# Optimization experiments

Hardware: AMD Instinct MI355X
Metric: run time of the kernel (lower is better)

Reference implementation:

```python
import jax, jax.numpy as jnp
import numpy as np

# ---- Cl(4,1) geometric-product Cayley table: gp(a,b)[k] = a[i] b[j] C[i,j,k] ----
def _build_cayley():
    metric = np.array([1.0, 1.0, 1.0, 1.0, -1.0], dtype=np.float32)  # signature (4,1)
    C = np.zeros((32, 32, 32), dtype=np.float32)
    for a in range(32):
        for b in range(32):
            # canonical reordering sign (count of swaps to merge blades)
            cnt = 0
            ash = a >> 1
            while ash:
                cnt += bin(ash & b).count('1')
                ash >>= 1
            s = -1.0 if (cnt & 1) else 1.0
            common = a & b
            for i in range(5):
                if (common >> i) & 1:
                    s *= metric[i]
            C[a, b, a ^ b] = s
    return C

CAYLEY = _build_cayley()
N_HEADS = 8

def gp_cl41(a, b, C):
    # a, b: (..., 32) multivectors
    return jnp.einsum('...i,...j,ijk->...k', a, b, C)

def normalize_cl41(x, eps=1e-6):
    n = jnp.sqrt(jnp.sum(x * x, axis=-1, keepdims=True) + eps)
    return x / n

def vlinear(x, w, b):
    # x: (..., Din, 32), w: (Dout, Din), b: (Dout, 32) -- blade-wise channel mixing
    return jnp.einsum('...ik,oi->...ok', x, w) + b

def layernorm2d(x, w, b, eps=1e-5):
    # normalized_shape = [D, 32]
    m = jnp.mean(x, axis=(-2, -1), keepdims=True)
    v = jnp.var(x, axis=(-2, -1), keepdims=True)
    return (x - m) / jnp.sqrt(v + eps) * w + b

def attention(x, wq, bq, wk, bk, wv, bv, wo, bo):
    B, S, D, K = x.shape
    hd = D // N_HEADS
    q = vlinear(x, wq, bq).reshape(B, S, N_HEADS, hd, K)
    k = vlinear(x, wk, bk).reshape(B, S, N_HEADS, hd, K)
    v = vlinear(x, wv, bv).reshape(B, S, N_HEADS, hd, K)
    scores = jnp.einsum('bqhdk,bshdk->bhqs', q, k) / jnp.sqrt(jnp.float32(hd * K))
    p = jax.nn.softmax(scores, axis=-1)
    o = jnp.einsum('bhqs,bshdk->bqhdk', p, v).reshape(B, S, D, K)
    return vlinear(o, wo, bo)


def setup_inputs() -> dict:
    key = jax.random.key(0)
    B, S, D, K = 4, 512, 256, 32
    L, E, NC = 2, 4, 1000
    ks = jax.random.split(key, 24)
    s = 1.0 / np.sqrt(D)
    inp = {
        'x': jax.random.normal(ks[0], (B, S, D, K), jnp.float32),
        'ln1_w': jnp.ones((L, D, K), jnp.float32),
        'ln1_b': jnp.zeros((L, D, K), jnp.float32),
        'wq': jax.random.normal(ks[1], (L, D, D), jnp.float32) * s,
        'bq': jnp.zeros((L, D, K), jnp.float32),
        'wk': jax.random.normal(ks[2], (L, D, D), jnp.float32) * s,
        'bk': jnp.zeros((L, D, K), jnp.float32),
        'wv': jax.random.normal(ks[3], (L, D, D), jnp.float32) * s,
        'bv': jnp.zeros((L, D, K), jnp.float32),
        'wo': jax.random.normal(ks[4], (L, D, D), jnp.float32) * s,
        'bo': jnp.zeros((L, D, K), jnp.float32),
        'ln2_w': jnp.ones((L, D, K), jnp.float32),
        'ln2_b': jnp.zeros((L, D, K), jnp.float32),
        'w1': jax.random.normal(ks[5], (L, E * D, D), jnp.float32) * s,
        'b1': jnp.zeros((L, E * D, K), jnp.float32),
        'w2': jax.random.normal(ks[6], (L, D, E * D), jnp.float32) * (1.0 / np.sqrt(E * D)),
        'b2': jnp.zeros((L, D, K), jnp.float32),
        'wr': jax.random.normal(ks[7], (D, D), jnp.float32) * s,
        'br': jnp.zeros((D, K), jnp.float32),
        'wc': jax.random.normal(ks[8], (NC, D * K), jnp.float32) * 0.02,
        'bc': jnp.zeros((NC,), jnp.float32),
    }
    return inp


def reference(x, ln1_w, ln1_b, wq, bq, wk, bk, wv, bv, wo, bo,
              ln2_w, ln2_b, w1, b1, w2, b2, wr, br, wc, bc):
    C = jnp.asarray(CAYLEY)
    L = ln1_w.shape[0]
    for l in range(L):
        h = layernorm2d(x, ln1_w[l], ln1_b[l])
        x = x + attention(h, wq[l], bq[l], wk[l], bk[l], wv[l], bv[l], wo[l], bo[l])
        x = normalize_cl41(x)
        h = layernorm2d(x, ln2_w[l], ln2_b[l])
        h = jnp.tanh(vlinear(h, w1[l], b1[l]))
        x = x + vlinear(h, w2[l], b2[l])
        x = normalize_cl41(x)
    # Recursive Rotor Accumulator pooling: psi_{t+1} = normalize(gp(r_t, psi_t))
    delta = vlinear(x, wr, br)                    # (B, S, D, 32)
    B, S, D, K = delta.shape
    psi0 = jnp.zeros((B, D, K), x.dtype).at[..., 0].set(1.0)
    def step(psi, r_t):
        return normalize_cl41(gp_cl41(r_t, psi, C)), None
    psi, _ = jax.lax.scan(step, psi0, jnp.moveaxis(delta, 1, 0))
    logits = psi.reshape(B, D * K) @ wc.T + bc
    return logits
```

## Files before the change

### kernel.cpp

```cpp
#include <hip/hip_runtime.h>
#include <hip/hip_bf16.h>
#include <cstdint>
#include <cstddef>

typedef __bf16 bf16_t;
typedef __attribute__((ext_vector_type(8))) __bf16 bf16x8;
typedef __attribute__((ext_vector_type(4))) __bf16 bf16x4;
typedef __attribute__((ext_vector_type(4))) float f32x4;

#define DEV __device__ __forceinline__

DEV void async16(const bf16_t* g, bf16_t* l) {
  __builtin_amdgcn_global_load_lds((const __attribute__((address_space(1))) void*)g,
                                   (__attribute__((address_space(3))) void*)l, 16, 0, 0);
}

DEV float fast_tanh(float x) {
  const float ex = __expf(2.f * x);
  return 1.f - 2.f / (ex + 1.f);
}

enum { EPI_RESID = 0, EPI_FFN1 = 1, EPI_QKV = 2, EPI_SCORE = 3, EPI_PV = 4, EPI_DELTAT = 5 };

template<int EPI, bool TRANSB>
__global__ __launch_bounds__(256, 2)
void gemm_k(const bf16_t* __restrict__ A, const bf16_t* __restrict__ A2,
            const bf16_t* __restrict__ B, const bf16_t* __restrict__ B2,
            const float* __restrict__ bias, void* __restrict__ outp, void* __restrict__ outp2,
            int Kd, int lda, int ldb, long aStride, long bStride)
{
  __shared__ bf16_t sA [2][4096];
  __shared__ bf16_t sB [2][4096];
  __shared__ bf16_t sA2[2][4096];
  __shared__ bf16_t sB2[2][4096];

  const int tid  = threadIdx.x;
  const int lane = tid & 63;
  const int wv   = tid >> 6;
  const int wr   = wv >> 1, wc = wv & 1;

  unsigned gx = gridDim.x, gy = gridDim.y;
  unsigned nb = gx * gy * gridDim.z;
  unsigned fid = blockIdx.x + gx * (blockIdx.y + gy * blockIdx.z);
  if ((nb & 7u) == 0u) fid = (fid & 7u) * (nb >> 3) + (fid >> 3);
  const unsigned bxu = fid % gx;
  const unsigned rem = fid / gx;
  const unsigned byu = rem % gy;
  const unsigned bzu = rem / gy;
  const int m0 = byu * 128;
  const int n0 = bxu * 128;
  const int bz = bzu;

  const bf16_t *Ab, *Bb, *A2b, *B2b;
  if constexpr (EPI == EPI_SCORE) {
    const int h = bz & 7;
    const long ho = (long)(bz >> 3) * 512;
    Ab  = A  + (long)h * aStride + ho;
    Bb  = B  + (long)h * bStride + ho;
    A2b = A2 + (long)h * aStride + ho;
    B2b = B2 + (long)h * bStride + ho;
  } else {
    Ab  = A  + (long)bz * aStride;
    Bb  = B  + (long)bz * bStride;
    A2b = A2 + (long)bz * aStride;
    B2b = B2 + (long)bz * bStride;
  }

  const int sRow = tid >> 2;
  const int sKo  = (tid & 3) * 8;
  const int tr = tid & 15;
  const int tc = tid >> 4;

  f32x4 acc[4][4];
#pragma unroll
  for (int i = 0; i < 4; i++)
#pragma unroll
    for (int j = 0; j < 4; j++) acc[i][j] = f32x4{0.f, 0.f, 0.f, 0.f};

  const int ns  = Kd >> 5;
  const int off = (int)(fid & (unsigned)(ns - 1));

  uint4 br0, br1, br2, br3;

  auto stageA = [&](int si, int b) {
    const int kt = ((si + off) & (ns - 1)) << 5;
    const bf16_t* ga  = Ab  + (long)(m0 + sRow) * lda + kt + sKo;
    const bf16_t* ga2 = A2b + (long)(m0 + sRow) * lda + kt + sKo;
    async16(ga,             &sA [b][tid * 8]);
    async16(ga + 64 * lda,  &sA [b][2048 + tid * 8]);
    async16(ga2,            &sA2[b][tid * 8]);
    async16(ga2 + 64 * lda, &sA2[b][2048 + tid * 8]);
  };
  auto stageB = [&](int si, int b) {
    const int kt = ((si + off) & (ns - 1)) << 5;
    const bf16_t* gb  = Bb  + (long)(n0 + sRow) * ldb + kt + sKo;
    const bf16_t* gb2 = B2b + (long)(n0 + sRow) * ldb + kt + sKo;
    async16(gb,             &sB [b][tid * 8]);
    async16(gb + 64 * ldb,  &sB [b][2048 + tid * 8]);
    async16(gb2,            &sB2[b][tid * 8]);
    async16(gb2 + 64 * ldb, &sB2[b][2048 + tid * 8]);
  };
  auto loadBR = [&](int si) {
    const int kt = ((si + off) & (ns - 1)) << 5;
    const bf16_t* gb  = Bb  + (long)(kt + tr) * ldb + n0 + tc * 8;
    const bf16_t* gb2 = B2b + (long)(kt + tr) * ldb + n0 + tc * 8;
    br0 = *(const uint4*)gb;
    br1 = *(const uint4*)(gb + 16 * ldb);
    br2 = *(const uint4*)gb2;
    br3 = *(const uint4*)(gb2 + 16 * ldb);
  };

  stageA(0, 0);
  if constexpr (!TRANSB) stageB(0, 0); else loadBR(0);

  for (int si = 0; si < ns; si++) {
    const int cb = si & 1;
    if (si + 1 < ns) stageA(si + 1, cb ^ 1);
    if constexpr (TRANSB) {
      const bf16_t* e0 = (const bf16_t*)&br0;
      const bf16_t* e1 = (const bf16_t*)&br1;
      const bf16_t* e2 = (const bf16_t*)&br2;
      const bf16_t* e3 = (const bf16_t*)&br3;
#pragma unroll
      for (int j = 0; j < 8; j++) {
        sB [cb][(tc * 8 + j) * 32 + tr]      = e0[j];
        sB [cb][(tc * 8 + j) * 32 + tr + 16] = e1[j];
        sB2[cb][(tc * 8 + j) * 32 + tr]      = e2[j];
        sB2[cb][(tc * 8 + j) * 32 + tr + 16] = e3[j];
      }
      if (si + 1 < ns) loadBR(si + 1);
      if (si + 1 >= ns) asm volatile("s_waitcnt vmcnt(0)" ::: "memory");
    } else {
      if (si + 1 < ns) {
        stageB(si + 1, cb ^ 1);
        asm volatile("s_waitcnt vmcnt(8)" ::: "memory");
      } else {
        asm volatile("s_waitcnt vmcnt(0)" ::: "memory");
      }
    }
    __syncthreads();

    bf16x8 af[4], bfr[4], af2[4], bf2[4];
#pragma unroll
    for (int i = 0; i < 4; i++) {
      const int ao = (wr * 64 + i * 16 + (lane & 15)) * 32 + (lane >> 4) * 8;
      const int bo = (wc * 64 + i * 16 + (lane & 15)) * 32 + (lane >> 4) * 8;
      af[i]  = *(const bf16x8*)&sA [cb][ao];
      af2[i] = *(const bf16x8*)&sA2[cb][ao];
      bfr[i] = *(const bf16x8*)&sB [cb][bo];
      bf2[i] = *(const bf16x8*)&sB2[cb][bo];
    }
#pragma unroll
    for (int i = 0; i < 4; i++)
#pragma unroll
      for (int j = 0; j < 4; j++) {
        acc[i][j] = __builtin_amdgcn_mfma_f32_16x16x32_bf16(af[i],  bfr[j], acc[i][j], 0, 0, 0);
        acc[i][j] = __builtin_amdgcn_mfma_f32_16x16x32_bf16(af[i],  bf2[j], acc[i][j], 0, 0, 0);
        acc[i][j] = __builtin_amdgcn_mfma_f32_16x16x32_bf16(af2[i], bfr[j], acc[i][j], 0, 0, 0);
      }
    __syncthreads();
  }

  const int cn = lane & 15;
  const int rg = (lane >> 4) * 4;
#pragma unroll
  for (int i = 0; i < 4; i++) {
    const int mb = m0 + wr * 64 + i * 16 + rg;
#pragma unroll
    for (int j = 0; j < 4; j++) {
      const int n = n0 + wc * 64 + j * 16 + cn;
#pragma unroll
      for (int r = 0; r < 4; r++) {
        const int m = mb + r;
        const float v = acc[i][j][r];
        if constexpr (EPI == EPI_RESID) {
          const float bb = bias ? bias[n * 32 + (m & 31)] : 0.f;
          ((float*)outp)[(long)m * 256 + n] += v + bb;
        } else if constexpr (EPI == EPI_QKV) {
          const int s = m >> 5, kb = m & 31;
          const int proj = n >> 8, col = n & 255;
          const int h = col >> 5, dd = col & 31;
          const long oidx = (long)proj * 4194304 + (long)(h * 512 + s) * 1024 + kb * 32 + dd;
          const float t = v + bias[n * 32 + kb];
          const bf16_t hh = (bf16_t)t;
          ((bf16_t*)outp)[oidx]  = hh;
          ((bf16_t*)outp2)[oidx] = (bf16_t)(t - (float)hh);
        } else if constexpr (EPI == EPI_SCORE) {
          const int h = bz & 7, half = bz >> 3;
          float* dst = half ? (float*)outp2 : (float*)outp;
          dst[(long)h * 262144 + (long)m * 512 + n] = v * (1.f / 32.f);
        } else if constexpr (EPI == EPI_PV) {
          const int kb = n >> 5, dd = n & 31;
          const long oidx = (long)(m * 32 + kb) * 256 + bz * 32 + dd;
          const bf16_t hh = (bf16_t)v;
          ((bf16_t*)outp)[oidx]  = hh;
          ((bf16_t*)outp2)[oidx] = (bf16_t)(v - (float)hh);
        } else {
          const int b = m >> 14, t = (m >> 5) & 511, kb = m & 31;
          ((float*)outp)[(((long)(b * 256 + n) * 512 + t) * 32) + kb] = v + bias[n * 32 + kb];
        }
      }
    }
  }
}

__global__ __launch_bounds__(256, 2)
void ffn_k(const bf16_t* __restrict__ Ah, const bf16_t* __restrict__ Al,
           const bf16_t* __restrict__ W1h_, const bf16_t* __restrict__ W1l_,
           const bf16_t* __restrict__ W2h_, const bf16_t* __restrict__ W2l_,
           const float* __restrict__ b1, const float* __restrict__ b2,
           float* __restrict__ XT)
{
  __shared__ bf16_t sAh[32 * 256], sAl[32 * 256];
  __shared__ bf16_t sHh[32 * 136], sHl[32 * 136];

  const int tid  = threadIdx.x;
  const int lane = tid & 63;
  const int wn   = tid >> 6;
  const int l15  = lane & 15;
  const int lg   = lane >> 4;
  const int m0   = blockIdx.x * 32;
  const int coff = blockIdx.x & 7;
  const int soff = (blockIdx.x >> 3) & 7;
  const int toff = (blockIdx.x >> 3) & 3;

#pragma unroll
  for (int r = 0; r < 4; r++) {
    const int idx = r * 256 + tid;
    const int row = idx >> 5, cp = idx & 31;
    const int c = cp ^ (row & 31);
    async16(Ah + (long)(m0 + row) * 256 + c * 8, sAh + idx * 8);
    async16(Al + (long)(m0 + row) * 256 + c * 8, sAl + idx * 8);
  }
  asm volatile("s_waitcnt vmcnt(0)" ::: "memory");
  __syncthreads();

  f32x4 acc2[2][4];
#pragma unroll
  for (int i = 0; i < 2; i++)
#pragma unroll
    for (int j = 0; j < 4; j++) acc2[i][j] = f32x4{0.f, 0.f, 0.f, 0.f};

#pragma unroll 1
  for (int cc = 0; cc < 8; cc++) {
    const int ch = (cc + coff) & 7;
    const bf16_t* W1h = W1h_ + (long)(ch * 128) * 256;
    const bf16_t* W1l = W1l_ + (long)(ch * 128) * 256;

    f32x4 acc1[2][2];
#pragma unroll
    for (int i = 0; i < 2; i++)
#pragma unroll
      for (int j = 0; j < 2; j++) acc1[i][j] = f32x4{0.f, 0.f, 0.f, 0.f};

#pragma unroll 2
    for (int s = 0; s < 8; s++) {
      const int sp = (s + soff) & 7;
      bf16x8 a_h[2], a_l[2], w_h[2], w_l[2];
#pragma unroll
      for (int i = 0; i < 2; i++) {
        const int arow = i * 16 + l15;
        const int ac = (sp * 4 + lg) ^ (arow & 31);
        a_h[i] = *(const bf16x8*)&sAh[arow * 256 + ac * 8];
        a_l[i] = *(const bf16x8*)&sAl[arow * 256 + ac * 8];
      }
#pragma unroll
      for (int j = 0; j < 2; j++) {
        const int nrow = wn * 32 + j * 16 + l15;
        w_h[j] = *(const bf16x8*)(W1h + (long)nrow * 256 + sp * 32 + lg * 8);
        w_l[j] = *(const bf16x8*)(W1l + (long)nrow * 256 + sp * 32 + lg * 8);
      }
#pragma unroll
      for (int i = 0; i < 2; i++)
#pragma unroll
        for (int j = 0; j < 2; j++) {
          acc1[i][j] = __builtin_amdgcn_mfma_f32_16x16x32_bf16(w_h[j], a_h[i], acc1[i][j], 0, 0, 0);
          acc1[i][j] = __builtin_amdgcn_mfma_f32_16x16x32_bf16(w_h[j], a_l[i], acc1[i][j], 0, 0, 0);
          acc1[i][j] = __builtin_amdgcn_mfma_f32_16x16x32_bf16(w_l[j], a_h[i], acc1[i][j], 0, 0, 0);
        }
    }

#pragma unroll
    for (int i = 0; i < 2; i++) {
      const int m = i * 16 + l15;
      const int kb = (m0 + m) & 31;
#pragma unroll
      for (int j = 0; j < 2; j++) {
        const int nb4 = wn * 32 + j * 16 + lg * 4;
        bf16x4 h4, l4;
#pragma unroll
        for (int rr = 0; rr < 4; rr++) {
          const int n = nb4 + rr;
          const float t = fast_tanh(acc1[i][j][rr] + b1[(ch * 128 + n) * 32 + kb]);
          const bf16_t hh = (bf16_t)t;
          h4[rr] = hh;
          l4[rr] = (bf16_t)(t - (float)hh);
        }
        *(bf16x4*)&sHh[m * 136 + nb4] = h4;
        *(bf16x4*)&sHl[m * 136 + nb4] = l4;
      }
    }
    __syncthreads();

#pragma unroll 2
    for (int t = 0; t < 4; t++) {
      const int tp = (t + toff) & 3;
      bf16x8 h_h[2], h_l[2], v_h[4], v_l[4];
#pragma unroll
      for (int i = 0; i < 2; i++) {
        const int hrow = i * 16 + l15;
        h_h[i] = *(const bf16x8*)&sHh[hrow * 136 + tp * 32 + lg * 8];
        h_l[i] = *(const bf16x8*)&sHl[hrow * 136 + tp * 32 + lg * 8];
      }
#pragma unroll
      for (int j = 0; j < 4; j++) {
        const int n2 = wn * 64 + j * 16 + l15;
        v_h[j] = *(const bf16x8*)(W2h_ + (long)n2 * 1024 + ch * 128 + tp * 32 + lg * 8);
        v_l[j] = *(const bf16x8*)(W2l_ + (long)n2 * 1024 + ch * 128 + tp * 32 + lg * 8);
      }
#pragma unroll
      for (int i = 0; i < 2; i++)
#pragma unroll
        for (int j = 0; j < 4; j++) {
          acc2[i][j] = __builtin_amdgcn_mfma_f32_16x16x32_bf16(h_h[i], v_h[j], acc2[i][j], 0, 0, 0);
          acc2[i][j] = __builtin_amdgcn_mfma_f32_16x16x32_bf16(h_h[i], v_l[j], acc2[i][j], 0, 0, 0);
          acc2[i][j] = __builtin_amdgcn_mfma_f32_16x16x32_bf16(h_l[i], v_h[j], acc2[i][j], 0, 0, 0);
        }
    }
    __syncthreads();
  }

#pragma unroll
  for (int i = 0; i < 2; i++)
#pragma unroll
    for (int j = 0; j < 4; j++) {
      const int n2 = wn * 64 + j * 16 + l15;
#pragma unroll
      for (int rr = 0; rr < 4; rr++) {
        const int m = m0 + i * 16 + lg * 4 + rr;
        XT[(long)m * 256 + n2] += acc2[i][j][rr] + b2[n2 * 32 + (m & 31)];
      }
    }
}

__global__ __launch_bounds__(256)
void transpose_k(const float* __restrict__ src, float* __restrict__ dst, int R, int C)
{
  __shared__ float t[32][33];
  const long boff = (long)blockIdx.z * R * C;
  const int r0 = blockIdx.y * 32, c0 = blockIdx.x * 32;
  const int tx = threadIdx.x & 31, ty = threadIdx.x >> 5;
#pragma unroll
  for (int i = 0; i < 32; i += 8)
    t[ty + i][tx] = src[boff + (long)(r0 + ty + i) * C + c0 + tx];
  __syncthreads();
#pragma unroll
  for (int i = 0; i < 32; i += 8)
    dst[boff + (long)(c0 + ty + i) * R + r0 + tx] = t[tx][ty + i];
}

DEV void hilo4(const f32x4 t, bf16x4& h, bf16x4& l) {
#pragma unroll
  for (int j = 0; j < 4; j++) {
    const bf16_t hh = (bf16_t)t[j];
    h[j] = hh;
    l[j] = (bf16_t)(t[j] - (float)hh);
  }
}

template<int MODE>
__global__ __launch_bounds__(256)
void nl_k(const float* __restrict__ X, float* __restrict__ Xo,
          const float* __restrict__ wT, const float* __restrict__ bT,
          bf16_t* __restrict__ oh, bf16_t* __restrict__ ol)
{
  const int row = blockIdx.x * 4 + (threadIdx.x >> 6);
  const int l   = threadIdx.x & 63;
  const float4* Xr = (const float4*)X + (long)row * 2048 + l;
  f32x4 v[32];
#pragma unroll
  for (int kb = 0; kb < 32; kb++) {
    const float4 t = Xr[kb * 64];
    v[kb] = f32x4{t.x, t.y, t.z, t.w};
  }
  if constexpr (MODE & 1) {
    f32x4 ss = f32x4{1e-6f, 1e-6f, 1e-6f, 1e-6f};
#pragma unroll
    for (int kb = 0; kb < 32; kb++) ss += v[kb] * v[kb];
    const f32x4 rs = f32x4{rsqrtf(ss[0]), rsqrtf(ss[1]), rsqrtf(ss[2]), rsqrtf(ss[3])};
#pragma unroll
    for (int kb = 0; kb < 32; kb++) v[kb] *= rs;
    if constexpr (MODE & 2) {
      float4* Xw = (float4*)Xo + (long)row * 2048 + l;
#pragma unroll
      for (int kb = 0; kb < 32; kb++)
        Xw[kb * 64] = float4{v[kb][0], v[kb][1], v[kb][2], v[kb][3]};
    }
  }
  if constexpr (MODE & 4) {
    float s = 0.f, s2 = 0.f;
#pragma unroll
    for (int kb = 0; kb < 32; kb++) {
      s  += (v[kb][0] + v[kb][1]) + (v[kb][2] + v[kb][3]);
      s2 += (v[kb][0] * v[kb][0] + v[kb][1] * v[kb][1]) +
            (v[kb][2] * v[kb][2] + v[kb][3] * v[kb][3]);
    }
#pragma unroll
    for (int o = 32; o > 0; o >>= 1) { s += __shfl_xor(s, o); s2 += __shfl_xor(s2, o); }
    const float mean = s * (1.f / 8192.f);
    const float var  = s2 * (1.f / 8192.f) - mean * mean;
    const float rstd = rsqrtf(var + 1e-5f);
    const float4* w4 = (const float4*)wT + l;
    const float4* b4 = (const float4*)bT + l;
#pragma unroll
    for (int kb = 0; kb < 32; kb++) {
      const float4 ww = w4[kb * 64];
      const float4 bb = b4[kb * 64];
      f32x4 t;
      t[0] = (v[kb][0] - mean) * rstd * ww.x + bb.x;
      t[1] = (v[kb][1] - mean) * rstd * ww.y + bb.y;
      t[2] = (v[kb][2] - mean) * rstd * ww.z + bb.z;
      t[3] = (v[kb][3] - mean) * rstd * ww.w + bb.w;
      bf16x4 h4, l4;
      hilo4(t, h4, l4);
      const long oi = (long)row * 8192 + kb * 256 + l * 4;
      *(bf16x4*)&oh[oi] = h4;
      *(bf16x4*)&ol[oi] = l4;
    }
  }
  if constexpr (MODE & 8) {
#pragma unroll
    for (int kb = 0; kb < 32; kb++) {
      bf16x4 h4, l4;
      hilo4(v[kb], h4, l4);
      const long oi = (long)row * 8192 + kb * 256 + l * 4;
      *(bf16x4*)&oh[oi] = h4;
      *(bf16x4*)&ol[oi] = l4;
    }
  }
}

__global__ __launch_bounds__(256)
void softmax_k(const float* __restrict__ SC, const float* __restrict__ SC2,
               bf16_t* __restrict__ Ph, bf16_t* __restrict__ Pl)
{
  const int row = blockIdx.x * 4 + (threadIdx.x >> 6);
  const int lane = threadIdx.x & 63;
  const float* s1 = SC  + (long)row * 512;
  const float* s2 = SC2 + (long)row * 512;
  float4 a = *(const float4*)&s1[lane * 4];
  float4 c = *(const float4*)&s1[256 + lane * 4];
  const float4 a2 = *(const float4*)&s2[lane * 4];
  const float4 c2 = *(const float4*)&s2[256 + lane * 4];
  a.x += a2.x; a.y += a2.y; a.z += a2.z; a.w += a2.w;
  c.x += c2.x; c.y += c2.y; c.z += c2.z; c.w += c2.w;
  float mx = fmaxf(fmaxf(fmaxf(a.x, a.y), fmaxf(a.z, a.w)),
                   fmaxf(fmaxf(c.x, c.y), fmaxf(c.z, c.w)));
#pragma unroll
  for (int o = 32; o > 0; o >>= 1) mx = fmaxf(mx, __shfl_xor(mx, o));
  float e[8] = {expf(a.x - mx), expf(a.y - mx), expf(a.z - mx), expf(a.w - mx),
                expf(c.x - mx), expf(c.y - mx), expf(c.z - mx), expf(c.w - mx)};
  float sum = ((e[0] + e[1]) + (e[2] + e[3])) + ((e[4] + e[5]) + (e[6] + e[7]));
#pragma unroll
  for (int o = 32; o > 0; o >>= 1) sum += __shfl_xor(sum, o);
  const float inv = 1.f / sum;
  bf16x4 h0, h1, l0, l1;
#pragma unroll
  for (int j = 0; j < 4; j++) {
    const float p0 = e[j] * inv, p1 = e[4 + j] * inv;
    h0[j] = (bf16_t)p0; l0[j] = (bf16_t)(p0 - (float)h0[j]);
    h1[j] = (bf16_t)p1; l1[j] = (bf16_t)(p1 - (float)h1[j]);
  }
  *(bf16x4*)&Ph[(long)row * 512 + lane * 4] = h0;
  *(bf16x4*)&Ph[(long)row * 512 + 256 + lane * 4] = h1;
  *(bf16x4*)&Pl[(long)row * 512 + lane * 4] = l0;
  *(bf16x4*)&Pl[(long)row * 512 + 256 + lane * 4] = l1;
}

constexpr float gpsign(int i, int j) {
  int cnt = 0;
  for (int s = 1; s < 5; s++) cnt += __builtin_popcount((i >> s) & j);
  float sgn = (cnt & 1) ? -1.f : 1.f;
  if ((i & j) & 16) sgn = -sgn;
  return sgn;
}

DEV void gp32(const float* __restrict__ a, const float* __restrict__ b, float* __restrict__ o) {
#pragma unroll
  for (int k = 0; k < 32; k++) {
    float s0 = 0.f, s1 = 0.f;
#pragma unroll
    for (int i = 0; i < 32; i += 2) {
      s0 = fmaf(gpsign(i, i ^ k) * a[i], b[i ^ k], s0);
      s1 = fmaf(gpsign(i + 1, (i + 1) ^ k) * a[i + 1], b[(i + 1) ^ k], s1);
    }
    o[k] = s0 + s1;
  }
}

__global__ __launch_bounds__(256)
void gptree_k(const float* __restrict__ dT, float* __restrict__ psiO)
{
  __shared__ float bufA[256 * 33];
  __shared__ float bufB[128 * 33];
  const int chain = blockIdx.x;
  const int t = threadIdx.x;
  const float* src = dT + (long)chain * (512 * 32);
  {
    float v[64];
    const float4* g = (const float4*)(src + t * 64);
#pragma unroll
    for (int i = 0; i < 16; i++) *(float4*)&v[i * 4] = g[i];
    float o[32];
    gp32(v + 32, v, o);
    float ss = 1e-6f;
#pragma unroll
    for (int k = 0; k < 32; k++) ss = fmaf(o[k], o[k], ss);
    const float rs = rsqrtf(ss);
#pragma unroll
    for (int k = 0; k < 32; k++) bufA[t * 33 + k] = o[k] * rs;
  }
  __syncthreads();
  int cur = 0;
#pragma unroll 1
  for (int P = 128; P >= 1; P >>= 1) {
    const float* in = cur ? bufB : bufA;
    float* ob = cur ? bufA : bufB;
    if (t < P) {
      float a[32], b[32], o[32];
#pragma unroll
      for (int c = 0; c < 32; c++) { b[c] = in[t * 66 + c]; a[c] = in[t * 66 + 33 + c]; }
      gp32(a, b, o);
      float ss = 1e-6f;
#pragma unroll
      for (int k = 0; k < 32; k++) ss = fmaf(o[k], o[k], ss);
      const float rs = rsqrtf(ss);
#pragma unroll
      for (int k = 0; k < 32; k++) ob[t * 33 + k] = o[k] * rs;
    }
    cur ^= 1;
    __syncthreads();
  }
  if (t < 32) psiO[(long)chain * 32 + t] = (cur ? bufB : bufA)[t];
}

__global__ __launch_bounds__(256)
void cls_k(const float* __restrict__ psi, const float* __restrict__ wcw,
           const float* __restrict__ bc, float* __restrict__ out)
{
  const int c = blockIdx.x;
  const int tid = threadIdx.x;
  float a0 = 0.f, a1 = 0.f, a2 = 0.f, a3 = 0.f;
  for (int i = tid * 4; i < 8192; i += 1024) {
    const float4 w  = *(const float4*)&wcw[(long)c * 8192 + i];
    const float4 p0 = *(const float4*)&psi[i];
    const float4 p1 = *(const float4*)&psi[8192 + i];
    const float4 p2 = *(const float4*)&psi[16384 + i];
    const float4 p3 = *(const float4*)&psi[24576 + i];
    a0 += w.x * p0.x + w.y * p0.y + w.z * p0.z + w.w * p0.w;
    a1 += w.x * p1.x + w.y * p1.y + w.z * p1.z + w.w * p1.w;
    a2 += w.x * p2.x + w.y * p2.y + w.z * p2.z + w.w * p2.w;
    a3 += w.x * p3.x + w.y * p3.y + w.z * p3.z + w.w * p3.w;
  }
#pragma unroll
  for (int o = 32; o > 0; o >>= 1) {
    a0 += __shfl_down(a0, o); a1 += __shfl_down(a1, o);
    a2 += __shfl_down(a2, o); a3 += __shfl_down(a3, o);
  }
  __shared__ float red[4][4];
  const int wv = tid >> 6;
  if ((tid & 63) == 0) { red[wv][0] = a0; red[wv][1] = a1; red[wv][2] = a2; red[wv][3] = a3; }
  __syncthreads();
  if (tid < 4) {
    const float r = red[0][tid] + red[1][tid] + red[2][tid] + red[3][tid] + bc[c];
    out[(long)tid * 1000 + c] = r;
  }
}

__global__ void split_k(const float* __restrict__ in, bf16_t* __restrict__ h,
                        bf16_t* __restrict__ l, int n)
{
  const int i = blockIdx.x * 256 + threadIdx.x;
  if (i < n) {
    const float v = in[i];
    const bf16_t hh = (bf16_t)v;
    h[i] = hh;
    l[i] = (bf16_t)(v - (float)hh);
  }
}

__global__ void cpy_k(const float* __restrict__ in, float* __restrict__ o, int n)
{
  const int i = blockIdx.x * 256 + threadIdx.x;
  if (i < n) o[i] = in[i];
}

extern "C" void kernel_launch(void* const* d_in, const int* in_sizes, int n_in,
                              void* d_out, int out_size, void* d_ws, size_t ws_size,
                              hipStream_t stream)
{
  const float* x    = (const float*)d_in[0];
  const float* ln1w = (const float*)d_in[1];
  const float* ln1b = (const float*)d_in[2];
  const float* wq   = (const float*)d_in[3];
  const float* bq   = (const float*)d_in[4];
  const float* wk   = (const float*)d_in[5];
  const float* bk   = (const float*)d_in[6];
  const float* wvv  = (const float*)d_in[7];
  const float* bv   = (const float*)d_in[8];
  const float* wo   = (const float*)d_in[9];
  const float* bo   = (const float*)d_in[10];
  const float* ln2w = (const float*)d_in[11];
  const float* ln2b = (const float*)d_in[12];
  const float* w1   = (const float*)d_in[13];
  const float* b1   = (const float*)d_in[14];
  const float* w2   = (const float*)d_in[15];
  const float* b2   = (const float*)d_in[16];
  const float* wr   = (const float*)d_in[17];
  const float* br   = (const float*)d_in[18];
  const float* wcw  = (const float*)d_in[19];
  const float* bc   = (const float*)d_in[20];
  float* out = (float*)d_out;

  char* ws = (char*)d_ws;
  const size_t MB = 1ull << 20;
  const size_t KB = 1024;
  float*  XT   = (float*)(ws + 0);
  bf16_t* HBh  = (bf16_t*)(ws + 64 * MB);
  bf16_t* HBl  = (bf16_t*)(ws + 96 * MB);
  bf16_t* QKVh = (bf16_t*)(ws + 128 * MB);
  bf16_t* QKVl = (bf16_t*)(ws + 152 * MB);
  float*  SCb  = (float*)(ws + 176 * MB);
  float*  SC2b = (float*)(ws + 184 * MB);
  bf16_t* Ph   = QKVh;
  bf16_t* Pl   = QKVl;
  bf16_t* OBh  = QKVh + 4194304;
  bf16_t* OBl  = QKVl + 4194304;
  bf16_t* Vh   = QKVh + 8388608;
  bf16_t* Vl   = QKVl + 8388608;
  bf16_t* XHI = (bf16_t*)(ws + 64 * MB), *XLO = (bf16_t*)(ws + 96 * MB);
  float*  DELTAT = (float*)(ws + 128 * MB);
  float*  PSI  = (float*)(ws + 192 * MB);
  char*   W    = ws + 193 * MB;
  bf16_t* WQKVh = (bf16_t*)(W);
  bf16_t* WQKVl = (bf16_t*)(W + 1 * MB);
  bf16_t* W1h = (bf16_t*)(W + 2 * MB);   bf16_t* W1l = (bf16_t*)(W + 3 * MB);
  bf16_t* W2h = (bf16_t*)(W + 4 * MB);   bf16_t* W2l = (bf16_t*)(W + 5 * MB);
  bf16_t* WOh = (bf16_t*)(W + 6 * MB);   bf16_t* WOl = (bf16_t*)(W + 6 * MB + 256 * KB);
  bf16_t* WRh = (bf16_t*)(W + 6 * MB + 512 * KB);
  bf16_t* WRl = (bf16_t*)(W + 6 * MB + 640 * KB);
  float*  BQKV = (float*)(W + 6 * MB + 768 * KB);
  float*  LNT  = (float*)(W + 6 * MB + 960 * KB);
  float* LN1WT = LNT, *LN1BT = LNT + 16384, *LN2WT = LNT + 32768, *LN2BT = LNT + 49152;

  for (int l = 0; l < 2; l++) {
    split_k<<<256, 256, 0, stream>>>(wq + l * 65536, WQKVh + l * 196608, WQKVl + l * 196608, 65536);
    split_k<<<256, 256, 0, stream>>>(wk + l * 65536, WQKVh + l * 196608 + 65536, WQKVl + l * 196608 + 65536, 65536);
    split_k<<<256, 256, 0, stream>>>(wvv + l * 65536, WQKVh + l * 196608 + 131072, WQKVl + l * 196608 + 131072, 65536);
    cpy_k<<<32, 256, 0, stream>>>(bq + l * 8192, BQKV + l * 24576, 8192);
    cpy_k<<<32, 256, 0, stream>>>(bk + l * 8192, BQKV + l * 24576 + 8192, 8192);
    cpy_k<<<32, 256, 0, stream>>>(bv + l * 8192, BQKV + l * 24576 + 16384, 8192);
  }
  split_k<<<512, 256, 0, stream>>>(wo, WOh, WOl, 131072);
  split_k<<<2048, 256, 0, stream>>>(w1, W1h, W1l, 524288);
  split_k<<<2048, 256, 0, stream>>>(w2, W2h, W2l, 524288);
  split_k<<<256, 256, 0, stream>>>(wr, WRh, WRl, 65536);
  transpose_k<<<dim3(1, 8, 2), 256, 0, stream>>>(ln1w, LN1WT, 256, 32);
  transpose_k<<<dim3(1, 8, 2), 256, 0, stream>>>(ln1b, LN1BT, 256, 32);
  transpose_k<<<dim3(1, 8, 2), 256, 0, stream>>>(ln2w, LN2WT, 256, 32);
  transpose_k<<<dim3(1, 8, 2), 256, 0, stream>>>(ln2b, LN2BT, 256, 32);

  transpose_k<<<dim3(1, 8, 2048), 256, 0, stream>>>(x, XT, 256, 32);

  for (int l = 0; l < 2; l++) {
    if (l == 0)
      nl_k<4><<<512, 256, 0, stream>>>(XT, nullptr, LN1WT, LN1BT, HBh, HBl);
    for (int b = 0; b < 4; b++) {
      const long ao = (long)b * 16384 * 256;
      gemm_k<EPI_QKV, false><<<dim3(6, 128, 1), 256, 0, stream>>>(
          HBh + ao, HBl + ao, WQKVh + l * 196608, WQKVl + l * 196608,
          BQKV + l * 24576, QKVh, QKVl, 256, 256, 256, 0, 0);
      gemm_k<EPI_SCORE, false><<<dim3(4, 4, 16), 256, 0, stream>>>(
          QKVh, QKVl, QKVh + 4194304, QKVl + 4194304,
          nullptr, SCb, SC2b, 512, 1024, 1024, 512 * 1024, 512 * 1024);
      softmax_k<<<1024, 256, 0, stream>>>(SCb, SC2b, Ph, Pl);
      gemm_k<EPI_PV, true><<<dim3(8, 4, 8), 256, 0, stream>>>(
          Ph, Pl, Vh, Vl, nullptr, OBh, OBl, 512, 512, 1024, 512 * 512, 512 * 1024);
      gemm_k<EPI_RESID, false><<<dim3(2, 128, 1), 256, 0, stream>>>(
          OBh, OBl, WOh + l * 65536, WOl + l * 65536,
          bo + l * 8192, (float*)XT + ao, nullptr, 256, 256, 256, 0, 0);
    }
    nl_k<1 | 2 | 4><<<512, 256, 0, stream>>>(XT, XT, LN2WT + l * 8192, LN2BT + l * 8192, HBh, HBl);
    ffn_k<<<2048, 256, 0, stream>>>(HBh, HBl,
                                    W1h + l * 262144, W1l + l * 262144,
                                    W2h + l * 262144, W2l + l * 262144,
                                    b1 + l * 32768, b2 + l * 8192, XT);
    if (l == 0) {
      nl_k<1 | 2 | 4><<<512, 256, 0, stream>>>(XT, XT, LN1WT + 8192, LN1BT + 8192, HBh, HBl);
    } else {
      nl_k<1 | 8><<<512, 256, 0, stream>>>(XT, nullptr, nullptr, nullptr, XHI, XLO);
    }
  }

  gemm_k<EPI_DELTAT, false><<<dim3(2, 512, 1), 256, 0, stream>>>(
      XHI, XLO, WRh, WRl, br, DELTAT, nullptr, 256, 256, 256, 0, 0);
  gptree_k<<<1024, 256, 0, stream>>>(DELTAT, PSI);
  cls_k<<<1000, 256, 0, stream>>>(PSI, wcw, bc, out);
}
```

Before: 2.295 ms.

## Stage FFN weight tiles through per-wave LDS buffers with async prefetch

The FFN kernel now loads W1 and W2 tiles into per-wave shared-memory buffers with async global-to-LDS copies. W1 is double-buffered so the next slice loads while the current one is consumed, and each W2 slice is prefetched after its registers are read. The H staging buffer also moves from a padded layout to an XOR-swizzled one to avoid bank conflicts. The aim is to hide global-load latency on the weights, at the cost of about 32KB more LDS and extra waitcnt stalls, which may lower occupancy below two blocks per CU.

```diff
diff --git a/kernel.cpp b/kernel.cpp
--- a/kernel.cpp
+++ b/kernel.cpp
@@ -212,7 +212,8 @@
            float* __restrict__ XT)
 {
   __shared__ bf16_t sAh[32 * 256], sAl[32 * 256];
-  __shared__ bf16_t sHh[32 * 136], sHl[32 * 136];
+  __shared__ bf16_t sW[4][4096];
+  __shared__ bf16_t sHh[32 * 128], sHl[32 * 128];
 
   const int tid  = threadIdx.x;
   const int lane = tid & 63;
@@ -235,6 +236,11 @@
   asm volatile("s_waitcnt vmcnt(0)" ::: "memory");
   __syncthreads();
 
+  bf16_t* myW = &sW[wn][0];
+  const int wrow1 = lane >> 2;
+  const int wsrc  = ((lane & 3) ^ ((lane >> 2) & 3)) * 8;
+  const int rpc   = (lg ^ (l15 & 3)) * 8;
+
   f32x4 acc2[2][4];
 #pragma unroll
   for (int i = 0; i < 2; i++)
@@ -247,15 +253,39 @@
     const bf16_t* W1h = W1h_ + (long)(ch * 128) * 256;
     const bf16_t* W1l = W1l_ + (long)(ch * 128) * 256;
 
+    auto stageW1 = [&](int sp, int b) {
+#pragma unroll
+      for (int q = 0; q < 2; q++) {
+        const long r = wn * 32 + q * 16 + wrow1;
+        async16(W1h + r * 256 + sp * 32 + wsrc, myW + b * 2048 + q * 512 + lane * 8);
+        async16(W1l + r * 256 + sp * 32 + wsrc, myW + b * 2048 + 1024 + q * 512 + lane * 8);
+      }
+    };
+    auto stageW2 = [&](int tp) {
+#pragma unroll
+      for (int q = 0; q < 4; q++) {
+        const long r = wn * 64 + q * 16 + wrow1;
+        async16(W2h_ + r * 1024 + ch * 128 + tp * 32 + wsrc, myW + q * 512 + lane * 8);
+        async16(W2l_ + r * 1024 + ch * 128 + tp * 32 + wsrc, myW + 2048 + q * 512 + lane * 8);
+      }
+    };
+
+    stageW1(soff & 7, 0);
     f32x4 acc1[2][2];
 #pragma unroll
     for (int i = 0; i < 2; i++)
 #pragma unroll
       for (int j = 0; j < 2; j++) acc1[i][j] = f32x4{0.f, 0.f, 0.f, 0.f};
 
-#pragma unroll 2
     for (int s = 0; s < 8; s++) {
+      const int b = s & 1;
       const int sp = (s + soff) & 7;
+      if (s < 7) {
+        stageW1((s + 1 + soff) & 7, b ^ 1);
+        asm volatile("s_waitcnt vmcnt(4)" ::: "memory");
+      } else {
+        asm volatile("s_waitcnt vmcnt(0)" ::: "memory");
+      }
       bf16x8 a_h[2], a_l[2], w_h[2], w_l[2];
 #pragma unroll
       for (int i = 0; i < 2; i++) {
@@ -266,9 +296,9 @@
       }
 #pragma unroll
       for (int j = 0; j < 2; j++) {
-        const int nrow = wn * 32 + j * 16 + l15;
-        w_h[j] = *(const bf16x8*)(W1h + (long)nrow * 256 + sp * 32 + lg * 8);
-        w_l[j] = *(const bf16x8*)(W1l + (long)nrow * 256 + sp * 32 + lg * 8);
+        const int r = j * 16 + l15;
+        w_h[j] = *(const bf16x8*)&myW[b * 2048 + r * 32 + rpc];
+        w_l[j] = *(const bf16x8*)&myW[b * 2048 + 1024 + r * 32 + rpc];
       }
 #pragma unroll
       for (int i = 0; i < 2; i++)
@@ -280,43 +310,53 @@
         }
     }
 
+    asm volatile("s_waitcnt lgkmcnt(0)" ::: "memory");
+    stageW2(toff & 3);
+
 #pragma unroll
     for (int i = 0; i < 2; i++) {
       const int m = i * 16 + l15;
       const int kb = (m0 + m) & 31;
 #pragma unroll
       for (int j = 0; j < 2; j++) {
-        const int nb4 = wn * 32 + j * 16 + lg * 4;
+        const int u = wn * 4 + j * 2 + (lg >> 1);
+        const int pu = u ^ (m & 7);
+        const int base = m * 128 + pu * 8 + (lg & 1) * 4;
+        const int ncol = wn * 32 + j * 16 + lg * 4;
         bf16x4 h4, l4;
 #pragma unroll
         for (int rr = 0; rr < 4; rr++) {
-          const int n = nb4 + rr;
-          const float t = fast_tanh(acc1[i][j][rr] + b1[(ch * 128 + n) * 32 + kb]);
+          const float t = fast_tanh(acc1[i][j][rr] + b1[(ch * 128 + ncol + rr) * 32 + kb]);
           const bf16_t hh = (bf16_t)t;
           h4[rr] = hh;
           l4[rr] = (bf16_t)(t - (float)hh);
         }
-        *(bf16x4*)&sHh[m * 136 + nb4] = h4;
-        *(bf16x4*)&sHl[m * 136 + nb4] = l4;
+        *(bf16x4*)&sHh[base] = h4;
+        *(bf16x4*)&sHl[base] = l4;
       }
     }
     __syncthreads();
 
-#pragma unroll 2
     for (int t = 0; t < 4; t++) {
       const int tp = (t + toff) & 3;
+      asm volatile("s_waitcnt vmcnt(0)" ::: "memory");
       bf16x8 h_h[2], h_l[2], v_h[4], v_l[4];
 #pragma unroll
       for (int i = 0; i < 2; i++) {
         const int hrow = i * 16 + l15;
-        h_h[i] = *(const bf16x8*)&sHh[hrow * 136 + tp * 32 + lg * 8];
-        h_l[i] = *(const bf16x8*)&sHl[hrow * 136 + tp * 32 + lg * 8];
+        const int pu = (tp * 4 + lg) ^ (hrow & 7);
+        h_h[i] = *(const bf16x8*)&sHh[hrow * 128 + pu * 8];
+        h_l[i] = *(const bf16x8*)&sHl[hrow * 128 + pu * 8];
       }
 #pragma unroll
       for (int j = 0; j < 4; j++) {
-        const int n2 = wn * 64 + j * 16 + l15;
-        v_h[j] = *(const bf16x8*)(W2h_ + (long)n2 * 1024 + ch * 128 + tp * 32 + lg * 8);
-        v_l[j] = *(const bf16x8*)(W2l_ + (long)n2 * 1024 + ch * 128 + tp * 32 + lg * 8);
+        const int r2 = j * 16 + l15;
+        v_h[j] = *(const bf16x8*)&myW[r2 * 32 + rpc];
+        v_l[j] = *(const bf16x8*)&myW[2048 + r2 * 32 + rpc];
+      }
+      if (t < 3) {
+        asm volatile("s_waitcnt lgkmcnt(0)" ::: "memory");
+        stageW2((t + 1 + toff) & 3);
       }
 #pragma unroll
       for (int i = 0; i < 2; i++)
```

After: 1.912 ms (median of 2 runs). 1.2x faster.
